# Kernel tuning notes

Hardware: AMD Instinct MI355X
Metric: run time of the kernel (lower is better)

## Reference

```python
import jax, jax.numpy as jnp
import numpy as np

EPS = 1e-6

def _rmsnorm(x, w):
    var = jnp.mean(x * x, axis=-1, keepdims=True)
    return x * jax.lax.rsqrt(var + EPS) * w

def _act_quant(x):
    # per-token int8 absmax quantization (BitNet b1.58)
    scale = 127.0 / jnp.clip(jnp.max(jnp.abs(x), axis=-1, keepdims=True), 1e-5)
    return jnp.round(jnp.clip(x * scale, -128.0, 127.0)) / scale

def _weight_quant(w):
    # per-tensor ternary quantization with mean-abs scale
    scale = 1.0 / jnp.clip(jnp.mean(jnp.abs(w)), 1e-5)
    return jnp.round(jnp.clip(w * scale, -1.0, 1.0)) / scale

def _ste(x, qfn):
    return x + jax.lax.stop_gradient(qfn(x) - x)

def _bitlinear(x, w):
    xq = _ste(x, _act_quant)
    wq = _ste(w, _weight_quant)
    return jnp.einsum('bsh,fh->bsf', xq, wq)

def setup_inputs() -> dict:
    key = jax.random.key(0)
    k1, k2, k3 = jax.random.split(key, 3)
    B, S, H, F = 4, 4096, 1024, 4096
    x = jax.random.normal(k1, (B, S, H), dtype=jnp.float32)
    norm_w = jnp.ones((H,), dtype=jnp.float32)
    w_up = jax.random.normal(k2, (F, H), dtype=jnp.float32) * (H ** -0.5)
    w_down = jax.random.normal(k3, (H, F), dtype=jnp.float32) * (F ** -0.5)
    return {"x": x, "norm_w": norm_w, "w_up": w_up, "w_down": w_down}

def reference(x, norm_w, w_up, w_down):
    residual = x
    h = _rmsnorm(x, norm_w)
    h = _bitlinear(h, w_up)          # [B,S,F]
    h = jnp.square(jax.nn.relu(h))   # relu^2
    h = _bitlinear(h, w_down)        # [B,S,H]
    return h + residual
```

## Files before the change

kernel.cpp:

```cpp
#include <hip/hip_runtime.h>
#include <hip/hip_fp16.h>

#define M_TOK 16384
#define H_DIM 1024
#define F_DIM 4096

typedef __attribute__((ext_vector_type(4))) int int4v;

static const size_t OFF_H2    = 0;
static const size_t OFF_Q2    = OFF_H2   + 134217728ULL;
static const size_t OFF_XQ    = OFF_Q2   + 67108864ULL;
static const size_t OFF_WQU   = OFF_XQ   + 16777216ULL;
static const size_t OFF_WQD   = OFF_WQU  + 4194304ULL;
static const size_t OFF_DQX   = OFF_WQD  + 4194304ULL;
static const size_t OFF_S2    = OFF_DQX  + 65536ULL;
static const size_t OFF_DQ2   = OFF_S2   + 65536ULL;
static const size_t OFF_PMAX  = OFF_DQ2  + 65536ULL;
static const size_t OFF_WPART = OFF_PMAX + 4194304ULL;
static const size_t OFF_WSC   = OFF_WPART+ 8192ULL;
static const size_t WS_NEEDED = OFF_WSC  + 16ULL;

__device__ __forceinline__ void ldg_lds16(const void* g, void* l) {
  __builtin_amdgcn_global_load_lds(
      (const __attribute__((address_space(1))) void*)g,
      (__attribute__((address_space(3))) void*)l, 16, 0, 0);
}

__global__ __launch_bounds__(256) void k_wabs(const float* __restrict__ wu,
                                              const float* __restrict__ wd,
                                              float* __restrict__ part) {
  const int b = blockIdx.x;
  const float* w = (b < 1024) ? wu : wd;
  const int cb = b & 1023;
  const size_t base = (size_t)cb * 4096 + threadIdx.x * 4;
  float s = 0.0f;
#pragma unroll
  for (int it = 0; it < 4; ++it) {
    const float4 v = *(const float4*)(w + base + it * 1024);
    s += fabsf(v.x) + fabsf(v.y) + fabsf(v.z) + fabsf(v.w);
  }
#pragma unroll
  for (int sh = 32; sh; sh >>= 1) s += __shfl_xor(s, sh, 64);
  __shared__ float red[4];
  if ((threadIdx.x & 63) == 0) red[threadIdx.x >> 6] = s;
  __syncthreads();
  if (threadIdx.x == 0) part[b] = red[0] + red[1] + red[2] + red[3];
}

__global__ __launch_bounds__(256) void k_wscale(const float* __restrict__ part,
                                                float* __restrict__ wsc) {
  const int b = blockIdx.x;
  const float* p = part + b * 1024;
  float s = p[threadIdx.x] + p[threadIdx.x + 256] + p[threadIdx.x + 512] + p[threadIdx.x + 768];
#pragma unroll
  for (int sh = 32; sh; sh >>= 1) s += __shfl_xor(s, sh, 64);
  __shared__ float red[4];
  if ((threadIdx.x & 63) == 0) red[threadIdx.x >> 6] = s;
  __syncthreads();
  if (threadIdx.x == 0) {
    const float mean = (red[0] + red[1] + red[2] + red[3]) * (1.0f / 4194304.0f);
    const float c = fmaxf(mean, 1e-5f);
    wsc[b * 2]     = c;
    wsc[b * 2 + 1] = 1.0f / c;
  }
}

__global__ __launch_bounds__(256) void k_wquant(const float* __restrict__ wu,
                                                const float* __restrict__ wd,
                                                char* __restrict__ qu,
                                                char* __restrict__ qd,
                                                const float* __restrict__ wsc) {
  const size_t t = (size_t)blockIdx.x * 256 + threadIdx.x;
  const float* w; char* q; float scale; size_t i;
  if (t < 1048576) { w = wu; q = qu; scale = wsc[1]; i = t * 4; }
  else             { w = wd; q = qd; scale = wsc[3]; i = (t - 1048576) * 4; }
  const float4 v = *(const float4*)(w + i);
  const int a = (int)rintf(fminf(fmaxf(v.x * scale, -1.0f), 1.0f));
  const int b = (int)rintf(fminf(fmaxf(v.y * scale, -1.0f), 1.0f));
  const int c = (int)rintf(fminf(fmaxf(v.z * scale, -1.0f), 1.0f));
  const int d = (int)rintf(fminf(fmaxf(v.w * scale, -1.0f), 1.0f));
  *(unsigned*)(q + i) = (a & 255) | ((b & 255) << 8) | ((c & 255) << 16) | ((d & 255) << 24);
}

__global__ __launch_bounds__(256) void k_rmsnorm_quant(const float* __restrict__ x,
                                                       const float* __restrict__ nw,
                                                       char* __restrict__ xq,
                                                       float* __restrict__ dqx) {
  const int row = blockIdx.x;
  const int t = threadIdx.x;
  const float4 v = *(const float4*)(x + (size_t)row * H_DIM + t * 4);
  float ss = v.x * v.x + v.y * v.y + v.z * v.z + v.w * v.w;
#pragma unroll
  for (int sh = 32; sh; sh >>= 1) ss += __shfl_xor(ss, sh, 64);
  __shared__ float red[4];
  __shared__ float redm[4];
  if ((t & 63) == 0) red[t >> 6] = ss;
  __syncthreads();
  ss = red[0] + red[1] + red[2] + red[3];
  const float rinv = 1.0f / sqrtf(ss * (1.0f / 1024.0f) + 1e-6f);
  const float4 w4 = *(const float4*)(nw + t * 4);
  float4 n;
  n.x = v.x * rinv * w4.x;  n.y = v.y * rinv * w4.y;
  n.z = v.z * rinv * w4.z;  n.w = v.w * rinv * w4.w;
  float am = fmaxf(fmaxf(fabsf(n.x), fabsf(n.y)), fmaxf(fabsf(n.z), fabsf(n.w)));
#pragma unroll
  for (int sh = 32; sh; sh >>= 1) am = fmaxf(am, __shfl_xor(am, sh, 64));
  if ((t & 63) == 0) redm[t >> 6] = am;
  __syncthreads();
  am = fmaxf(fmaxf(redm[0], redm[1]), fmaxf(redm[2], redm[3]));
  am = fmaxf(am, 1e-5f);
  const float scale = 127.0f / am;
  const int qa = (int)rintf(fminf(fmaxf(n.x * scale, -128.0f), 127.0f));
  const int qb = (int)rintf(fminf(fmaxf(n.y * scale, -128.0f), 127.0f));
  const int qc = (int)rintf(fminf(fmaxf(n.z * scale, -128.0f), 127.0f));
  const int qd = (int)rintf(fminf(fmaxf(n.w * scale, -128.0f), 127.0f));
  *(unsigned*)(xq + (size_t)row * H_DIM + t * 4) =
      (qa & 255) | ((qb & 255) << 8) | ((qc & 255) << 16) | ((qd & 255) << 24);
  if (t == 0) dqx[row] = am * (1.0f / 127.0f);
}

template <int LDA_, int LDB_, int KTILES>
__device__ __forceinline__ void gemm_core(const char* __restrict__ A,
                                          const char* __restrict__ B,
                                          int mBase, int nBase,
                                          char* As, char* Bs, int4v acc[4][4]) {
  const int t = threadIdx.x;
  const int lane = t & 63;
  const int wm = (t >> 6) & 1;
  const int wn = t >> 7;
  const int sRow = t >> 2;
  const int sSeg = (((t & 3) ^ ((t >> 3) & 3)) << 4);
  const char* Ag0 = A + (size_t)(mBase + sRow) * LDA_ + sSeg;
  const char* Ag1 = A + (size_t)(mBase + 64 + sRow) * LDA_ + sSeg;
  const char* Bg0 = B + (size_t)(nBase + sRow) * LDB_ + sSeg;
  const char* Bg1 = B + (size_t)(nBase + 64 + sRow) * LDB_ + sSeg;
  char* Al0 = As + t * 16;
  char* Al1 = As + 4096 + t * 16;
  char* Bl0 = Bs + t * 16;
  char* Bl1 = Bs + 4096 + t * 16;
  const int q = lane >> 4;
  const int r0a = wm * 64 + (lane & 15);
  const int r0b = wn * 64 + (lane & 15);
  const int aOff = r0a * 64 + ((q ^ ((r0a >> 1) & 3)) << 4);
  const int bOff = r0b * 64 + ((q ^ ((r0b >> 1) & 3)) << 4);

  for (int kt = 0; kt < KTILES; ++kt) {
    __syncthreads();
    ldg_lds16(Ag0, Al0);
    ldg_lds16(Ag1, Al1);
    ldg_lds16(Bg0, Bl0);
    ldg_lds16(Bg1, Bl1);
    Ag0 += 64; Ag1 += 64; Bg0 += 64; Bg1 += 64;
    __syncthreads();
    int4v a[4], b[4];
#pragma unroll
    for (int i = 0; i < 4; ++i) a[i] = *(const int4v*)(As + aOff + i * 16 * 64);
#pragma unroll
    for (int j = 0; j < 4; ++j) b[j] = *(const int4v*)(Bs + bOff + j * 16 * 64);
#pragma unroll
    for (int i = 0; i < 4; ++i)
#pragma unroll
      for (int j = 0; j < 4; ++j)
        acc[i][j] = __builtin_amdgcn_mfma_i32_16x16x64_i8(a[i], b[j], acc[i][j], 0, 0, 0);
  }
}

__global__ __launch_bounds__(256, 2) void k_gemm1(const char* __restrict__ xq,
                                                  const char* __restrict__ wq,
                                                  const float* __restrict__ wsc,
                                                  const float* __restrict__ dqx,
                                                  __half* __restrict__ h2,
                                                  float* __restrict__ pmax) {
  __shared__ char smem[16384];
  int4v acc[4][4];
#pragma unroll
  for (int i = 0; i < 4; ++i)
#pragma unroll
    for (int j = 0; j < 4; ++j) acc[i][j] = (int4v){0, 0, 0, 0};
  const int mBase = blockIdx.x * 128;
  const int nBase = blockIdx.y * 128;
  gemm_core<H_DIM, H_DIM, 16>(xq, wq, mBase, nBase, smem, smem + 8192, acc);

  const int t = threadIdx.x;
  const int lane = t & 63;
  const int wm = (t >> 6) & 1;
  const int wn = t >> 7;
  const float dqw = wsc[0];
#pragma unroll
  for (int i = 0; i < 4; ++i) {
    const int rbase = mBase + wm * 64 + i * 16 + ((lane >> 4) << 2);
    const float4 dq4 = *(const float4*)(dqx + rbase);
    const float* dqp = (const float*)&dq4;
    float rmax[4] = {0.0f, 0.0f, 0.0f, 0.0f};
#pragma unroll
    for (int j = 0; j < 4; ++j) {
      const int col = nBase + wn * 64 + j * 16 + (lane & 15);
#pragma unroll
      for (int r = 0; r < 4; ++r) {
        float v = (float)acc[i][j][r] * dqp[r] * dqw;
        v = fmaxf(v, 0.0f);
        v = v * v;
        const __half h = __float2half(v);
        h2[(size_t)(rbase + r) * F_DIM + col] = h;
        rmax[r] = fmaxf(rmax[r], __half2float(h));
      }
    }
#pragma unroll
    for (int s = 1; s < 16; s <<= 1) {
#pragma unroll
      for (int r = 0; r < 4; ++r) rmax[r] = fmaxf(rmax[r], __shfl_xor(rmax[r], s, 64));
    }
    if ((lane & 15) == 0) {
      const int nb2 = blockIdx.y * 2 + wn;
#pragma unroll
      for (int r = 0; r < 4; ++r) pmax[(size_t)nb2 * M_TOK + rbase + r] = rmax[r];
    }
  }
}

__global__ __launch_bounds__(256) void k_rowred(const float* __restrict__ pmax,
                                                float* __restrict__ scale2,
                                                float* __restrict__ dq2) {
  const int row = blockIdx.x * 256 + threadIdx.x;
  float m = 0.0f;
#pragma unroll
  for (int i = 0; i < 64; ++i) m = fmaxf(m, pmax[(size_t)i * M_TOK + row]);
  m = fmaxf(m, 1e-5f);
  scale2[row] = 127.0f / m;
  dq2[row] = m * (1.0f / 127.0f);
}

__global__ __launch_bounds__(256) void k_quant2(const __half* __restrict__ h2,
                                                const float* __restrict__ scale2,
                                                char* __restrict__ q2) {
  const size_t t = (size_t)blockIdx.x * 256 + threadIdx.x;
  const size_t i = t * 8;
  const int row = (int)(i >> 12);
  const float s = scale2[row];
  __half2 hh[4];
  *(float4*)hh = *(const float4*)(h2 + i);
  int q[8];
#pragma unroll
  for (int k = 0; k < 4; ++k) {
    const float lo = __low2float(hh[k]);
    const float hi = __high2float(hh[k]);
    q[2 * k]     = (int)rintf(fminf(lo * s, 127.0f));
    q[2 * k + 1] = (int)rintf(fminf(hi * s, 127.0f));
  }
  const unsigned u0 = (q[0] & 255) | ((q[1] & 255) << 8) | ((q[2] & 255) << 16) | ((q[3] & 255) << 24);
  const unsigned u1 = (q[4] & 255) | ((q[5] & 255) << 8) | ((q[6] & 255) << 16) | ((q[7] & 255) << 24);
  *(uint2*)(q2 + i) = make_uint2(u0, u1);
}

__global__ __launch_bounds__(256, 2) void k_gemm2(const char* __restrict__ q2,
                                                  const char* __restrict__ wq,
                                                  const float* __restrict__ wsc,
                                                  const float* __restrict__ dq2,
                                                  const float* __restrict__ x,
                                                  float* __restrict__ out) {
  __shared__ char smem[16384];
  int4v acc[4][4];
#pragma unroll
  for (int i = 0; i < 4; ++i)
#pragma unroll
    for (int j = 0; j < 4; ++j) acc[i][j] = (int4v){0, 0, 0, 0};
  const int mBase = blockIdx.x * 128;
  const int nBase = blockIdx.y * 128;
  gemm_core<F_DIM, F_DIM, 64>(q2, wq, mBase, nBase, smem, smem + 8192, acc);

  const int t = threadIdx.x;
  const int lane = t & 63;
  const int wm = (t >> 6) & 1;
  const int wn = t >> 7;
  const float dqw = wsc[2];
#pragma unroll
  for (int i = 0; i < 4; ++i) {
    const int rbase = mBase + wm * 64 + i * 16 + ((lane >> 4) << 2);
    const float4 dq4 = *(const float4*)(dq2 + rbase);
    const float* dqp = (const float*)&dq4;
#pragma unroll
    for (int j = 0; j < 4; ++j) {
      const int col = nBase + wn * 64 + j * 16 + (lane & 15);
#pragma unroll
      for (int r = 0; r < 4; ++r) {
        const size_t idx = (size_t)(rbase + r) * H_DIM + col;
        out[idx] = (float)acc[i][j][r] * dqp[r] * dqw + x[idx];
      }
    }
  }
}

extern "C" void kernel_launch(void* const* d_in, const int* in_sizes, int n_in,
                              void* d_out, int out_size, void* d_ws, size_t ws_size,
                              hipStream_t stream) {
  const float* x  = (const float*)d_in[0];
  const float* nw = (const float*)d_in[1];
  const float* wu = (const float*)d_in[2];
  const float* wd = (const float*)d_in[3];
  float* out = (float*)d_out;
  char* ws = (char*)d_ws;
  if (ws_size < WS_NEEDED) return;

  __half* h2     = (__half*)(ws + OFF_H2);
  char* q2       = ws + OFF_Q2;
  char* xq       = ws + OFF_XQ;
  char* wqu      = ws + OFF_WQU;
  char* wqd      = ws + OFF_WQD;
  float* dqx     = (float*)(ws + OFF_DQX);
  float* scale2  = (float*)(ws + OFF_S2);
  float* dq2     = (float*)(ws + OFF_DQ2);
  float* pmax    = (float*)(ws + OFF_PMAX);
  float* wpart   = (float*)(ws + OFF_WPART);
  float* wsc     = (float*)(ws + OFF_WSC);

  k_wabs<<<2048, 256, 0, stream>>>(wu, wd, wpart);
  k_wscale<<<2, 256, 0, stream>>>(wpart, wsc);
  k_wquant<<<8192, 256, 0, stream>>>(wu, wd, wqu, wqd, wsc);
  k_rmsnorm_quant<<<M_TOK, 256, 0, stream>>>(x, nw, xq, dqx);
  k_gemm1<<<dim3(M_TOK / 128, F_DIM / 128), 256, 0, stream>>>(xq, wqu, wsc, dqx, h2, pmax);
  k_rowred<<<M_TOK / 256, 256, 0, stream>>>(pmax, scale2, dq2);
  k_quant2<<<(M_TOK * (F_DIM / 8)) / 256, 256, 0, stream>>>(h2, scale2, q2);
  k_gemm2<<<dim3(M_TOK / 128, H_DIM / 128), 256, 0, stream>>>(q2, wqd, wsc, dq2, x, out);
}
```

Measured before the change: 385.8 us.

## Double GEMM K-tile depth to 128 and fuse row-max reduction into quant2

The shared GEMM core now stages 128-byte K slices per iteration instead of 64, with an 8-way XOR swizzle. This halves the number of barrier pairs per tile and runs two MFMA sub-steps per load phase, which raises LDS use to 32 KB per block. Separately, the per-row max reduction over partial maxima is folded into the second quantization kernel, launched one block per row with a wave shuffle reduction. That removes one launch and the scale2 buffer round trip.

Measured after the change: 361.4 us. 1.07x faster.

```diff
diff --git a/kernel.cpp b/kernel.cpp
--- a/kernel.cpp
+++ b/kernel.cpp
@@ -13,8 +13,7 @@
 static const size_t OFF_WQU   = OFF_XQ   + 16777216ULL;
 static const size_t OFF_WQD   = OFF_WQU  + 4194304ULL;
 static const size_t OFF_DQX   = OFF_WQD  + 4194304ULL;
-static const size_t OFF_S2    = OFF_DQX  + 65536ULL;
-static const size_t OFF_DQ2   = OFF_S2   + 65536ULL;
+static const size_t OFF_DQ2   = OFF_DQX  + 65536ULL;
 static const size_t OFF_PMAX  = OFF_DQ2  + 65536ULL;
 static const size_t OFF_WPART = OFF_PMAX + 4194304ULL;
 static const size_t OFF_WSC   = OFF_WPART+ 8192ULL;
@@ -128,40 +127,41 @@
   const int lane = t & 63;
   const int wm = (t >> 6) & 1;
   const int wn = t >> 7;
-  const int sRow = t >> 2;
-  const int sSeg = (((t & 3) ^ ((t >> 3) & 3)) << 4);
-  const char* Ag0 = A + (size_t)(mBase + sRow) * LDA_ + sSeg;
-  const char* Ag1 = A + (size_t)(mBase + 64 + sRow) * LDA_ + sSeg;
-  const char* Bg0 = B + (size_t)(nBase + sRow) * LDB_ + sSeg;
-  const char* Bg1 = B + (size_t)(nBase + 64 + sRow) * LDB_ + sSeg;
-  char* Al0 = As + t * 16;
-  char* Al1 = As + 4096 + t * 16;
-  char* Bl0 = Bs + t * 16;
-  char* Bl1 = Bs + 4096 + t * 16;
+  const int sRow = t >> 3;
+  const int sSeg = (t & 7) ^ (sRow & 7);
+  const char* Ag = A + (size_t)(mBase + sRow) * LDA_ + sSeg * 16;
+  const char* Bg = B + (size_t)(nBase + sRow) * LDB_ + sSeg * 16;
+  char* Al = As + t * 16;
+  char* Bl = Bs + t * 16;
   const int q = lane >> 4;
-  const int r0a = wm * 64 + (lane & 15);
-  const int r0b = wn * 64 + (lane & 15);
-  const int aOff = r0a * 64 + ((q ^ ((r0a >> 1) & 3)) << 4);
-  const int bOff = r0b * 64 + ((q ^ ((r0b >> 1) & 3)) << 4);
+  const int rA = wm * 64 + (lane & 15);
+  const int rB = wn * 64 + (lane & 15);
+  const int swA = rA & 7;
+  const int swB = rB & 7;
 
   for (int kt = 0; kt < KTILES; ++kt) {
     __syncthreads();
-    ldg_lds16(Ag0, Al0);
-    ldg_lds16(Ag1, Al1);
-    ldg_lds16(Bg0, Bl0);
-    ldg_lds16(Bg1, Bl1);
-    Ag0 += 64; Ag1 += 64; Bg0 += 64; Bg1 += 64;
+#pragma unroll
+    for (int n = 0; n < 4; ++n) ldg_lds16(Ag + (size_t)n * 32 * LDA_, Al + n * 4096);
+#pragma unroll
+    for (int n = 0; n < 4; ++n) ldg_lds16(Bg + (size_t)n * 32 * LDB_, Bl + n * 4096);
+    Ag += 128; Bg += 128;
     __syncthreads();
-    int4v a[4], b[4];
-#pragma unroll
-    for (int i = 0; i < 4; ++i) a[i] = *(const int4v*)(As + aOff + i * 16 * 64);
-#pragma unroll
-    for (int j = 0; j < 4; ++j) b[j] = *(const int4v*)(Bs + bOff + j * 16 * 64);
-#pragma unroll
-    for (int i = 0; i < 4; ++i)
-#pragma unroll
-      for (int j = 0; j < 4; ++j)
-        acc[i][j] = __builtin_amdgcn_mfma_i32_16x16x64_i8(a[i], b[j], acc[i][j], 0, 0, 0);
+#pragma unroll
+    for (int ks = 0; ks < 2; ++ks) {
+      const int ao = (((ks * 4 + q) ^ swA) << 4);
+      const int bo = (((ks * 4 + q) ^ swB) << 4);
+      int4v a[4], b[4];
+#pragma unroll
+      for (int i = 0; i < 4; ++i) a[i] = *(const int4v*)(As + (rA + i * 16) * 128 + ao);
+#pragma unroll
+      for (int j = 0; j < 4; ++j) b[j] = *(const int4v*)(Bs + (rB + j * 16) * 128 + bo);
+#pragma unroll
+      for (int i = 0; i < 4; ++i)
+#pragma unroll
+        for (int j = 0; j < 4; ++j)
+          acc[i][j] = __builtin_amdgcn_mfma_i32_16x16x64_i8(a[i], b[j], acc[i][j], 0, 0, 0);
+    }
   }
 }
 
@@ -171,7 +171,7 @@
                                                   const float* __restrict__ dqx,
                                                   __half* __restrict__ h2,
                                                   float* __restrict__ pmax) {
-  __shared__ char smem[16384];
+  __shared__ char smem[32768];
   int4v acc[4][4];
 #pragma unroll
   for (int i = 0; i < 4; ++i)
@@ -179,7 +179,7 @@
     for (int j = 0; j < 4; ++j) acc[i][j] = (int4v){0, 0, 0, 0};
   const int mBase = blockIdx.x * 128;
   const int nBase = blockIdx.y * 128;
-  gemm_core<H_DIM, H_DIM, 16>(xq, wq, mBase, nBase, smem, smem + 8192, acc);
+  gemm_core<H_DIM, H_DIM, 8>(xq, wq, mBase, nBase, smem, smem + 16384, acc);
 
   const int t = threadIdx.x;
   const int lane = t & 63;
@@ -218,38 +218,37 @@
   }
 }
 
-__global__ __launch_bounds__(256) void k_rowred(const float* __restrict__ pmax,
-                                                float* __restrict__ scale2,
+__global__ __launch_bounds__(256) void k_quant2(const __half* __restrict__ h2,
+                                                const float* __restrict__ pmax,
+                                                char* __restrict__ q2,
                                                 float* __restrict__ dq2) {
-  const int row = blockIdx.x * 256 + threadIdx.x;
-  float m = 0.0f;
-#pragma unroll
-  for (int i = 0; i < 64; ++i) m = fmaxf(m, pmax[(size_t)i * M_TOK + row]);
-  m = fmaxf(m, 1e-5f);
-  scale2[row] = 127.0f / m;
-  dq2[row] = m * (1.0f / 127.0f);
-}
-
-__global__ __launch_bounds__(256) void k_quant2(const __half* __restrict__ h2,
-                                                const float* __restrict__ scale2,
-                                                char* __restrict__ q2) {
-  const size_t t = (size_t)blockIdx.x * 256 + threadIdx.x;
-  const size_t i = t * 8;
-  const int row = (int)(i >> 12);
-  const float s = scale2[row];
-  __half2 hh[4];
-  *(float4*)hh = *(const float4*)(h2 + i);
-  int q[8];
+  const int row = blockIdx.x;
+  const int t = threadIdx.x;
+  __shared__ float sm;
+  if (t < 64) {
+    float m = pmax[(size_t)t * M_TOK + row];
+#pragma unroll
+    for (int sh = 32; sh; sh >>= 1) m = fmaxf(m, __shfl_xor(m, sh, 64));
+    if (t == 0) sm = fmaxf(m, 1e-5f);
+  }
+  __syncthreads();
+  const float mx = sm;
+  const float s = 127.0f / mx;
+  if (t == 0) dq2[row] = mx * (1.0f / 127.0f);
+  const size_t i = (size_t)row * F_DIM + t * 16;
+  __half2 hh[8];
+  *(float4*)(hh)     = *(const float4*)(h2 + i);
+  *(float4*)(hh + 4) = *(const float4*)(h2 + i + 8);
+  unsigned u[4];
 #pragma unroll
   for (int k = 0; k < 4; ++k) {
-    const float lo = __low2float(hh[k]);
-    const float hi = __high2float(hh[k]);
-    q[2 * k]     = (int)rintf(fminf(lo * s, 127.0f));
-    q[2 * k + 1] = (int)rintf(fminf(hi * s, 127.0f));
-  }
-  const unsigned u0 = (q[0] & 255) | ((q[1] & 255) << 8) | ((q[2] & 255) << 16) | ((q[3] & 255) << 24);
-  const unsigned u1 = (q[4] & 255) | ((q[5] & 255) << 8) | ((q[6] & 255) << 16) | ((q[7] & 255) << 24);
-  *(uint2*)(q2 + i) = make_uint2(u0, u1);
+    const int q0 = (int)rintf(fminf(__low2float(hh[2 * k]) * s, 127.0f));
+    const int q1 = (int)rintf(fminf(__high2float(hh[2 * k]) * s, 127.0f));
+    const int q2i = (int)rintf(fminf(__low2float(hh[2 * k + 1]) * s, 127.0f));
+    const int q3 = (int)rintf(fminf(__high2float(hh[2 * k + 1]) * s, 127.0f));
+    u[k] = (q0 & 255) | ((q1 & 255) << 8) | ((q2i & 255) << 16) | ((q3 & 255) << 24);
+  }
+  *(uint4*)(q2 + i) = make_uint4(u[0], u[1], u[2], u[3]);
 }
 
 __global__ __launch_bounds__(256, 2) void k_gemm2(const char* __restrict__ q2,
@@ -258,7 +257,7 @@
                                                   const float* __restrict__ dq2,
                                                   const float* __restrict__ x,
                                                   float* __restrict__ out) {
-  __shared__ char smem[16384];
+  __shared__ char smem[32768];
   int4v acc[4][4];
 #pragma unroll
   for (int i = 0; i < 4; ++i)
@@ -266,7 +265,7 @@
     for (int j = 0; j < 4; ++j) acc[i][j] = (int4v){0, 0, 0, 0};
   const int mBase = blockIdx.x * 128;
   const int nBase = blockIdx.y * 128;
-  gemm_core<F_DIM, F_DIM, 64>(q2, wq, mBase, nBase, smem, smem + 8192, acc);
+  gemm_core<F_DIM, F_DIM, 32>(q2, wq, mBase, nBase, smem, smem + 16384, acc);
 
   const int t = threadIdx.x;
   const int lane = t & 63;
@@ -307,7 +306,6 @@
   char* wqu      = ws + OFF_WQU;
   char* wqd      = ws + OFF_WQD;
   float* dqx     = (float*)(ws + OFF_DQX);
-  float* scale2  = (float*)(ws + OFF_S2);
   float* dq2     = (float*)(ws + OFF_DQ2);
   float* pmax    = (float*)(ws + OFF_PMAX);
   float* wpart   = (float*)(ws + OFF_WPART);
@@ -318,7 +316,6 @@
   k_wquant<<<8192, 256, 0, stream>>>(wu, wd, wqu, wqd, wsc);
   k_rmsnorm_quant<<<M_TOK, 256, 0, stream>>>(x, nw, xq, dqx);
   k_gemm1<<<dim3(M_TOK / 128, F_DIM / 128), 256, 0, stream>>>(xq, wqu, wsc, dqx, h2, pmax);
-  k_rowred<<<M_TOK / 256, 256, 0, stream>>>(pmax, scale2, dq2);
-  k_quant2<<<(M_TOK * (F_DIM / 8)) / 256, 256, 0, stream>>>(h2, scale2, q2);
+  k_quant2<<<M_TOK, 256, 0, stream>>>(h2, pmax, q2, dq2);
   k_gemm2<<<dim3(M_TOK / 128, H_DIM / 128), 256, 0, stream>>>(q2, wqd, wsc, dq2, x, out);
 }
```
